# Kernel tuning notes

Measured on AMD Instinct MI355X. Metric: run time of the kernel, lower is better.

Reference implementation:

```python
import jax, jax.numpy as jnp
import numpy as np

G = 16                 # grid side -> 4096 voxels
N_GRID = G ** 3
N_NODES = 4096         # protein nodes
DEG = 256              # node neighbors per grid voxel
HID = 64               # MPNN hidden == ResNet in_channels
NUM_CLASSES = 20
BN = np.float32(1.0 / np.sqrt(1.0 + 1e-5))  # eval-mode BatchNorm3d (mean=0, var=1, gamma=1, beta=0)


def _lin(key, fi, fo):
    return jax.random.normal(key, (fi, fo), jnp.float32) * (fi ** -0.5)


def _cw(key, o, i, k):
    return jax.random.normal(key, (o, i, k, k, k), jnp.float32) * ((i * k ** 3) ** -0.5)


def setup_inputs() -> dict:
    key = jax.random.key(0)
    ks = jax.random.split(key, 32)
    n_edges = N_GRID * DEG
    # every grid voxel receives exactly DEG messages (bincount never zero)
    edge_i = jax.random.randint(ks[0], (n_edges,), 0, N_NODES, dtype=jnp.int32)
    edge_j = jnp.repeat(jnp.arange(N_GRID, dtype=jnp.int32), DEG)
    edge_index = jnp.stack([edge_i, edge_j])  # [2, E]

    node_embedding = jax.random.normal(ks[1], (N_NODES, HID), jnp.float32)
    node_pos = jax.random.uniform(ks[2], (N_NODES, 3), jnp.float32)
    gx = (jnp.arange(G, dtype=jnp.float32) + 0.5) / G
    gd, gh, gw = jnp.meshgrid(gx, gx, gx, indexing='ij')
    grid_pos = jnp.stack([gd, gh, gw], -1).reshape(N_GRID, 3)

    z = lambda n: jnp.zeros((n,), jnp.float32)
    return {
        'node_embedding': node_embedding, 'node_pos': node_pos,
        'grid_pos': grid_pos, 'edge_index': edge_index,
        # MPNN edge / message / update MLPs
        'ew1': _lin(ks[3], 6, HID), 'eb1': z(HID), 'ew2': _lin(ks[4], HID, HID), 'eb2': z(HID),
        'mw1': _lin(ks[5], 2 * HID, HID), 'mb1': z(HID), 'mw2': _lin(ks[6], HID, HID), 'mb2': z(HID),
        'uw1': _lin(ks[7], HID, HID), 'ub1': z(HID), 'uw2': _lin(ks[8], HID, HID), 'ub2': z(HID),
        # ResNet3D: 3 Blocks (conv3 a, conv3 b, conv5 shortcut) with channels 64->64, 64->128, 128->256
        'c1a': _cw(ks[9], 64, 64, 3), 'c1b': _cw(ks[10], 64, 64, 3), 'c1s': _cw(ks[11], 64, 64, 5),
        'c2a': _cw(ks[12], 128, 64, 3), 'c2b': _cw(ks[13], 128, 128, 3), 'c2s': _cw(ks[14], 128, 64, 5),
        'c3a': _cw(ks[15], 256, 128, 3), 'c3b': _cw(ks[16], 256, 256, 3), 'c3s': _cw(ks[17], 256, 128, 5),
        'fcw': _lin(ks[18], 256, NUM_CLASSES), 'fcb': z(NUM_CLASSES),
    }


def _mlp(x, w1, b1, w2, b2):
    return jax.nn.silu(x @ w1 + b1) @ w2 + b2


def _conv(x, w, p):
    return jax.lax.conv_general_dilated(
        x, w, window_strides=(1, 1, 1), padding=[(p, p)] * 3,
        dimension_numbers=('NCDHW', 'OIDHW', 'NCDHW'))


def _block(x, wa, wb, ws):
    out = jax.nn.relu(_conv(x, wa, 1) * BN)
    out = _conv(out, wb, 1) * BN
    sc = _conv(x, ws, 2) * BN
    return jax.nn.relu(out + sc)


def reference(node_embedding, node_pos, grid_pos, edge_index,
              ew1, eb1, ew2, eb2, mw1, mb1, mw2, mb2, uw1, ub1, uw2, ub2,
              c1a, c1b, c1s, c2a, c2b, c2s, c3a, c3b, c3s, fcw, fcb):
    i, j = edge_index[0], edge_index[1]
    # ---- MPNN: gather, edge MLP, message MLP, scatter-mean, update MLP ----
    edge_attr = jnp.concatenate([node_pos[i], grid_pos[j]], axis=-1)        # [E, 6]
    pos_emb = _mlp(edge_attr, ew1, eb1, ew2, eb2)                           # [E, H]
    msg = _mlp(jnp.concatenate([node_embedding[i], pos_emb], -1),
               mw1, mb1, mw2, mb2)                                          # [E, H]
    agg = jax.ops.segment_sum(msg, j, num_segments=N_GRID)                  # [N_GRID, H]
    cnt = jax.ops.segment_sum(jnp.ones((msg.shape[0],), msg.dtype), j,
                              num_segments=N_GRID)
    grid_feat = _mlp(agg / cnt[:, None], uw1, ub1, uw2, ub2)                # [N_GRID, H]
    # ---- ResNet3D over the grid volume ----
    x = grid_feat.T.reshape(1, HID, G, G, G) * BN                           # instance_norm1 (eval BN)
    x = _block(x, c1a, c1b, c1s)
    x = _block(x, c2a, c2b, c2s)
    x = _block(x, c3a, c3b, c3s)
    pooled = jnp.max(x, axis=(2, 3, 4))                                     # max_pool3d(kernel=spatial)
    return pooled @ fcw + fcb                                               # [1, NUM_CLASSES]
```

## Files before the change

kernel.cpp:

```cpp
#include <hip/hip_runtime.h>
#include <math.h>

#define BN_S 0.9999950000374997f

typedef _Float16 half8 __attribute__((ext_vector_type(8)));
typedef float f32x4 __attribute__((ext_vector_type(4)));

__device__ __forceinline__ float silu_f(float x) {
    return __fdividef(x, 1.0f + __expf(-x));
}

__device__ __forceinline__ void gld16(const void* g, void* l) {
    __builtin_amdgcn_global_load_lds(
        (const __attribute__((address_space(1))) void*)g,
        (__attribute__((address_space(3))) void*)l, 16, 0, 0);
}

__global__ __launch_bounds__(64) void prep_w_k(
    const float* __restrict__ ew2, const float* __restrict__ mw1,
    const float* __restrict__ mw2, const float* __restrict__ uw1,
    const float* __restrict__ mb2, const float* __restrict__ ub1,
    float* __restrict__ W_mu, float* __restrict__ b_mu,
    _Float16* __restrict__ wemt_h, _Float16* __restrict__ wemt_l)
{
    const int k = blockIdx.x, c = threadIdx.x;
    float s = 0.f;
    for (int m = 0; m < 64; m++) s = fmaf(ew2[k*64 + m], mw1[(64 + m)*64 + c], s);
    {
        const int q = k >> 5, kg = (k >> 3) & 3, jj = k & 7;
        const int sl = q*256 + c*4 + kg;
        const int p = sl ^ ((sl >> 3) & 7);
        const _Float16 h = (_Float16)s;
        const _Float16 l = (_Float16)(s - (float)h);
        wemt_h[p*8 + jj] = h;
        wemt_l[p*8 + jj] = l;
    }
    float s2 = 0.f;
    for (int m = 0; m < 64; m++) s2 = fmaf(mw2[k*64 + m], uw1[m*64 + c], s2);
    W_mu[k*64 + c] = s2;
    if (k == 0) {
        float s3 = ub1[c];
        for (int m = 0; m < 64; m++) s3 = fmaf(mb2[m], uw1[m*64 + c], s3);
        b_mu[c] = s3;
    }
}

__global__ __launch_bounds__(64) void prep_nodes_k(
    const float* __restrict__ node_embedding, const float* __restrict__ node_pos,
    const float* __restrict__ grid_pos, const float* __restrict__ ew1,
    const float* __restrict__ eb1, const float* __restrict__ mw1,
    const float* __restrict__ mb1, const float* __restrict__ eb2,
    float* __restrict__ a_node, float* __restrict__ g_vox, float* __restrict__ n_node)
{
    const int v = blockIdx.x, c = threadIdx.x;
    const float p0 = node_pos[v*3], p1 = node_pos[v*3 + 1], p2 = node_pos[v*3 + 2];
    a_node[v*64 + c] = fmaf(p0, ew1[c], fmaf(p1, ew1[64 + c], fmaf(p2, ew1[128 + c], eb1[c])));
    const float q0 = grid_pos[v*3], q1 = grid_pos[v*3 + 1], q2 = grid_pos[v*3 + 2];
    g_vox[v*64 + c] = fmaf(q0, ew1[192 + c], fmaf(q1, ew1[256 + c], q2 * ew1[320 + c]));
    float s = mb1[c];
    for (int k = 0; k < 64; k++) s = fmaf(node_embedding[v*64 + k], mw1[k*64 + c], s);
    for (int k = 0; k < 64; k++) s = fmaf(eb2[k], mw1[(64 + k)*64 + c], s);
    n_node[v*64 + c] = s;
}

template<int K3, int NCOG, int NCH>
__global__ __launch_bounds__(256) void wsplit_k(
    const float* __restrict__ w, _Float16* __restrict__ dh, _Float16* __restrict__ dl,
    int CI)
{
    __shared__ float s[32*K3];
    const int co = blockIdx.x, cig = blockIdx.y, t = threadIdx.x;
    const float* src = w + ((size_t)co*CI + cig*32)*K3;
    for (int m = t; m < 32*K3; m += 256) s[m] = src[m];
    __syncthreads();
    const int coG = co >> 6, col = co & 63;
    for (int m = t; m < 32*K3; m += 256) {
        const int tap = m >> 5, cil = m & 31;
        const float x = s[cil*K3 + tap];
        const _Float16 h = (_Float16)x;
        const _Float16 l = (_Float16)(x - (float)h);
        const int b = cil >> 3, jj = cil & 7;
        const int sl = col*4 + b;
        const int p = sl ^ ((sl >> 3) & 7);
        const size_t base = ((size_t)(tap*NCOG + coG)*NCH + cig) * 2048;
        dh[base + p*8 + jj] = h;
        dl[base + p*8 + jj] = l;
    }
}

__global__ __launch_bounds__(256) void edge_kernel(
    const int* __restrict__ edge_i,
    const float* __restrict__ a_node, const float* __restrict__ g_vox,
    const float* __restrict__ n_node,
    const _Float16* __restrict__ wemt_h, const _Float16* __restrict__ wemt_l,
    const float* __restrict__ W_mu, const float* __restrict__ b_mu,
    const float* __restrict__ uw2, const float* __restrict__ ub2,
    _Float16* __restrict__ x0h, _Float16* __restrict__ x0l)
{
    __shared__ __align__(16) _Float16 sAh[4096], sAl[4096];
    __shared__ __align__(16) _Float16 sBh[4096], sBl[4096];
    __shared__ float sV1[64], sV2[64];

    const int j = blockIdx.x, t = threadIdx.x;
    const int lane = t & 63, wv = t >> 6, ln15 = lane & 15, kg = lane >> 4;
    const int ebase = j << 8;

    gld16(wemt_h + t*8, &sAh[t*8]);
    gld16(wemt_h + 2048 + t*8, &sAh[2048 + t*8]);
    gld16(wemt_l + t*8, &sAl[t*8]);
    gld16(wemt_l + 2048 + t*8, &sAl[2048 + t*8]);

    const int r = t >> 2, sub = t & 3;
    float gv[16];
    #pragma unroll
    for (int m = 0; m < 16; m++) gv[m] = g_vox[j*64 + sub*16 + m];

    asm volatile("s_waitcnt vmcnt(0)" ::: "memory");
    __syncthreads();

    float psum[4] = {0.f, 0.f, 0.f, 0.f};

    for (int T = 0; T < 4; T++) {
        {
            const int i = edge_i[ebase + T*64 + r];
            float s1[16];
            #pragma unroll
            for (int m = 0; m < 16; m++)
                s1[m] = silu_f(a_node[i*64 + sub*16 + m] + gv[m]);
            half8 h0, l0, h1, l1;
            #pragma unroll
            for (int m = 0; m < 8; m++) {
                h0[m] = (_Float16)s1[m];
                l0[m] = (_Float16)(s1[m] - (float)h0[m]);
                h1[m] = (_Float16)s1[8 + m];
                l1[m] = (_Float16)(s1[8 + m] - (float)h1[m]);
            }
            const int q = sub >> 1, kg0 = (sub & 1) * 2;
            const int slot0 = (q*4 + kg0)*64 + r;
            *(half8*)&sBh[slot0*8] = h0; *(half8*)&sBl[slot0*8] = l0;
            *(half8*)&sBh[(slot0 + 64)*8] = h1; *(half8*)&sBl[(slot0 + 64)*8] = l1;
        }
        __syncthreads();
        #pragma unroll
        for (int eF = 0; eF < 4; eF++) {
            const int e = eF*16 + ln15;
            const int ie = edge_i[ebase + T*64 + e];
            f32x4 acc;
            {
                const float4 nv = *(const float4*)&n_node[(size_t)ie*64 + wv*16 + kg*4];
                acc[0] = nv.x; acc[1] = nv.y; acc[2] = nv.z; acc[3] = nv.w;
            }
            #pragma unroll
            for (int q = 0; q < 2; q++) {
                const int sa = q*256 + (wv*16 + ln15)*4 + kg;
                const int pa = sa ^ ((sa >> 3) & 7);
                const half8 Ah = *(const half8*)&sAh[pa*8];
                const half8 Al = *(const half8*)&sAl[pa*8];
                const int sb = ((q*4 + kg)*64 + e)*8;
                const half8 Bh = *(const half8*)&sBh[sb];
                const half8 Bl = *(const half8*)&sBl[sb];
                acc = __builtin_amdgcn_mfma_f32_16x16x32_f16(Ah, Bh, acc, 0, 0, 0);
                acc = __builtin_amdgcn_mfma_f32_16x16x32_f16(Ah, Bl, acc, 0, 0, 0);
                acc = __builtin_amdgcn_mfma_f32_16x16x32_f16(Al, Bh, acc, 0, 0, 0);
            }
            #pragma unroll
            for (int rg = 0; rg < 4; rg++) psum[rg] += silu_f(acc[rg]);
        }
        __syncthreads();
    }

    #pragma unroll
    for (int rg = 0; rg < 4; rg++) {
        float v = psum[rg];
        v += __shfl_xor(v, 1, 64); v += __shfl_xor(v, 2, 64);
        v += __shfl_xor(v, 4, 64); v += __shfl_xor(v, 8, 64);
        psum[rg] = v;
    }
    if (ln15 == 0) {
        #pragma unroll
        for (int rg = 0; rg < 4; rg++)
            sV1[wv*16 + kg*4 + rg] = psum[rg] * (1.0f / 256.0f);
    }
    __syncthreads();
    if (t < 64) {
        float h = b_mu[t];
        for (int k = 0; k < 64; k++) h = fmaf(sV1[k], W_mu[k*64 + t], h);
        sV2[t] = silu_f(h);
    }
    __syncthreads();
    if (t < 64) {
        float g = ub2[t];
        for (int k = 0; k < 64; k++) g = fmaf(sV2[k], uw2[k*64 + t], g);
        const float val = g * BN_S;
        const _Float16 hh = (_Float16)val;
        const _Float16 ll = (_Float16)(val - (float)hh);
        const int c = t, zz = j >> 8, v = j & 255;
        const size_t a16 = ((size_t)((c >> 5)*16 + zz)*1024 + ((c >> 3) & 3)*256 + v)*8 + (c & 7);
        x0h[a16] = hh; x0l[a16] = ll;
    }
}

template<int KK, int CI, int NCO32, int CIS>
__global__ __launch_bounds__(256) void conv_mfma_k(
    const _Float16* __restrict__ xh, const _Float16* __restrict__ xl,
    const _Float16* __restrict__ wh, const _Float16* __restrict__ wl,
    float* __restrict__ slab)
{
    constexpr int P = KK/2, K2 = KK*KK, NCH = CI/32, NCHS = NCH/CIS;
    constexpr int CO = NCO32*32, NCOG64 = NCO32/2;
    const int d0 = blockIdx.x, coG32 = blockIdx.y;
    const int co64G = coG32 >> 1, coHalf = coG32 & 1;
    const int cis = blockIdx.z / KK, kd = blockIdx.z % KK;
    const int t = threadIdx.x;
    const int lane = t & 63, wv = t >> 6;
    const int ln15 = lane & 15, kg = lane >> 4;

    float* sout = slab + ((size_t)blockIdx.z*CO + coG32*32)*4096 + d0*256;
    const int z = d0 + kd - P;
    if ((unsigned)z >= 16u) {
        for (int m = t; m < 32*256; m += 256)
            sout[(size_t)(m >> 8)*4096 + (m & 255)] = 0.f;
        return;
    }

    __shared__ __align__(16) _Float16 sXh[2][8192];
    __shared__ __align__(16) _Float16 sXl[2][8192];
    __shared__ __align__(16) _Float16 zb[8];
    if (t < 8) zb[t] = (_Float16)0.f;

    int aoff[2];
    #pragma unroll
    for (int cf = 0; cf < 2; cf++) {
        const int s = (coHalf*32 + cf*16 + ln15)*4 + kg;
        aoff[cf] = (s ^ ((s >> 3) & 7)) * 8;
    }

    auto stage_X = [&](int xb, int ch) {
        const size_t b16 = ((size_t)ch*16 + z) * 8192;
        #pragma unroll
        for (int q = 0; q < 4; q++) {
            gld16(xh + b16 + (q*256 + t)*8, &sXh[xb][(q*256 + t)*8]);
            gld16(xl + b16 + (q*256 + t)*8, &sXl[xb][(q*256 + t)*8]);
        }
    };
    auto loadA = [&](int ch, int t2, half8* Ah, half8* Al) {
        const size_t b = ((size_t)((kd*K2 + t2)*NCOG64 + co64G)*NCH + ch) * 2048;
        #pragma unroll
        for (int cf = 0; cf < 2; cf++) {
            Ah[cf] = *(const half8*)&wh[b + aoff[cf]];
            Al[cf] = *(const half8*)&wl[b + aoff[cf]];
        }
    };

    f32x4 acc[2][4];
    #pragma unroll
    for (int a = 0; a < 2; a++)
        #pragma unroll
        for (int b = 0; b < 4; b++)
            #pragma unroll
            for (int r2 = 0; r2 < 4; r2++) acc[a][b][r2] = 0.f;

    const int ch0 = cis * NCHS;
    half8 nAh[2], nAl[2];
    stage_X(0, ch0);
    loadA(ch0, 0, nAh, nAl);
    asm volatile("s_waitcnt vmcnt(0)" ::: "memory");
    __syncthreads();

    for (int cc = 0; cc < NCHS; cc++) {
        const int ch = ch0 + cc, xb = cc & 1;
        if (cc + 1 < NCHS) stage_X(xb ^ 1, ch + 1);
        for (int t2 = 0; t2 < K2; t2++) {
            half8 cAh[2], cAl[2];
            #pragma unroll
            for (int cf = 0; cf < 2; cf++) { cAh[cf] = nAh[cf]; cAl[cf] = nAl[cf]; }
            if (t2 + 1 < K2)          loadA(ch, t2 + 1, nAh, nAl);
            else if (cc + 1 < NCHS)   loadA(ch + 1, 0, nAh, nAl);

            const int kh = t2 / KK, kw = t2 % KK;
            __builtin_amdgcn_s_setprio(1);
            #pragma unroll
            for (int f = 0; f < 4; f++) {
                const int h_in = wv*4 + f + kh - P;
                if ((unsigned)h_in < 16u) {
                    const int w_in = ln15 + kw - P;
                    const bool ok = (unsigned)w_in < 16u;
                    const int slot = ok ? (kg*256 + h_in*16 + w_in) : 0;
                    const half8 Bh = ok ? *(const half8*)&sXh[xb][slot*8] : *(const half8*)zb;
                    const half8 Bl = ok ? *(const half8*)&sXl[xb][slot*8] : *(const half8*)zb;
                    #pragma unroll
                    for (int cf = 0; cf < 2; cf++) {
                        acc[cf][f] = __builtin_amdgcn_mfma_f32_16x16x32_f16(cAh[cf], Bh, acc[cf][f], 0, 0, 0);
                        acc[cf][f] = __builtin_amdgcn_mfma_f32_16x16x32_f16(cAh[cf], Bl, acc[cf][f], 0, 0, 0);
                        acc[cf][f] = __builtin_amdgcn_mfma_f32_16x16x32_f16(cAl[cf], Bh, acc[cf][f], 0, 0, 0);
                    }
                }
            }
            __builtin_amdgcn_s_setprio(0);
        }
        asm volatile("s_waitcnt vmcnt(0)" ::: "memory");
        __syncthreads();
    }

    #pragma unroll
    for (int cf = 0; cf < 2; cf++)
        #pragma unroll
        for (int f = 0; f < 4; f++)
            #pragma unroll
            for (int r2 = 0; r2 < 4; r2++)
                sout[(size_t)(cf*16 + kg*4 + r2)*4096 + wv*64 + f*16 + ln15] = acc[cf][f][r2];
}

template<int S, int RMODE, int OUT>
__global__ __launch_bounds__(256) void reduce_k(
    const float* __restrict__ pbuf, const float* __restrict__ addsrc,
    float* __restrict__ outf, _Float16* __restrict__ oh, _Float16* __restrict__ ol,
    int CO)
{
    const int z = blockIdx.x, c8 = blockIdx.y, v = threadIdx.x;
    float val[8];
    #pragma unroll
    for (int jj = 0; jj < 8; jj++) {
        const int c = c8*8 + jj;
        float a = 0.f;
        #pragma unroll
        for (int s = 0; s < S; s++)
            a += pbuf[((size_t)s*CO + c)*4096 + z*256 + v];
        a *= BN_S;
        if (RMODE == 3) a += addsrc[(size_t)c*4096 + z*256 + v];
        if (RMODE != 2) a = fmaxf(a, 0.f);
        val[jj] = a;
    }
    if (OUT == 0) {
        #pragma unroll
        for (int jj = 0; jj < 8; jj++)
            outf[(size_t)(c8*8 + jj)*4096 + z*256 + v] = val[jj];
    } else if (OUT == 1) {
        half8 hv, lv;
        #pragma unroll
        for (int jj = 0; jj < 8; jj++) {
            hv[jj] = (_Float16)val[jj];
            lv[jj] = (_Float16)(val[jj] - (float)hv[jj]);
        }
        const size_t a16 = ((size_t)((c8 >> 2)*16 + z)*1024 + (c8 & 3)*256 + v)*8;
        *(half8*)&oh[a16] = hv;
        *(half8*)&ol[a16] = lv;
    } else {
        __shared__ float sm[4][8];
        #pragma unroll
        for (int jj = 0; jj < 8; jj++) {
            float m = val[jj];
            m = fmaxf(m, __shfl_xor(m, 1, 64));  m = fmaxf(m, __shfl_xor(m, 2, 64));
            m = fmaxf(m, __shfl_xor(m, 4, 64));  m = fmaxf(m, __shfl_xor(m, 8, 64));
            m = fmaxf(m, __shfl_xor(m, 16, 64)); m = fmaxf(m, __shfl_xor(m, 32, 64));
            if ((v & 63) == 0) sm[v >> 6][jj] = m;
        }
        __syncthreads();
        if (v < 8) {
            const float m = fmaxf(fmaxf(sm[0][v], sm[1][v]), fmaxf(sm[2][v], sm[3][v]));
            outf[z*CO + c8*8 + v] = m;
        }
    }
}

__global__ __launch_bounds__(256) void fc_k(
    const float* __restrict__ pp, const float* __restrict__ fcw,
    const float* __restrict__ fcb, float* __restrict__ out)
{
    __shared__ float sp[256];
    const int t = threadIdx.x;
    float m = pp[t];
    for (int zz = 1; zz < 16; zz++) m = fmaxf(m, pp[zz*256 + t]);
    sp[t] = m;
    __syncthreads();
    if (t < 20) {
        float s = fcb[t];
        for (int c = 0; c < 256; c++) s = fmaf(sp[c], fcw[c*20 + t], s);
        out[t] = s;
    }
}

extern "C" void kernel_launch(void* const* d_in, const int* in_sizes, int n_in,
                              void* d_out, int out_size, void* d_ws, size_t ws_size,
                              hipStream_t stream)
{
    const float* node_embedding = (const float*)d_in[0];
    const float* node_pos       = (const float*)d_in[1];
    const float* grid_pos       = (const float*)d_in[2];
    const int*   edge_index     = (const int*)d_in[3];
    const float* ew1 = (const float*)d_in[4];
    const float* eb1 = (const float*)d_in[5];
    const float* ew2 = (const float*)d_in[6];
    const float* eb2 = (const float*)d_in[7];
    const float* mw1 = (const float*)d_in[8];
    const float* mb1 = (const float*)d_in[9];
    const float* mw2 = (const float*)d_in[10];
    const float* mb2 = (const float*)d_in[11];
    const float* uw1 = (const float*)d_in[12];
    const float* ub1 = (const float*)d_in[13];
    const float* uw2 = (const float*)d_in[14];
    const float* ub2 = (const float*)d_in[15];
    const float* c1a = (const float*)d_in[16];
    const float* c1b = (const float*)d_in[17];
    const float* c1s = (const float*)d_in[18];
    const float* c2a = (const float*)d_in[19];
    const float* c2b = (const float*)d_in[20];
    const float* c2s = (const float*)d_in[21];
    const float* c3a = (const float*)d_in[22];
    const float* c3b = (const float*)d_in[23];
    const float* c3s = (const float*)d_in[24];
    const float* fcw = (const float*)d_in[25];
    const float* fcb = (const float*)d_in[26];
    float* out = (float*)d_out;
    const int* edge_i = edge_index;

    float* ws = (float*)d_ws;
    float* a_node = ws;                ws += 262144;
    float* g_vox  = ws;                ws += 262144;
    float* n_node = ws;                ws += 262144;
    float* W_mu   = ws;                ws += 4096;
    float* b_mu   = ws;                ws += 64;
    _Float16* wemt_h = (_Float16*)ws;  ws += 2048;
    _Float16* wemt_l = (_Float16*)ws;  ws += 2048;
    _Float16* x0h = (_Float16*)ws;     ws += 131072;
    _Float16* x0l = (_Float16*)ws;     ws += 131072;
    _Float16* t2h = (_Float16*)ws;     ws += 262144;
    _Float16* t2l = (_Float16*)ws;     ws += 262144;
    _Float16* x2h = (_Float16*)ws;     ws += 262144;
    _Float16* x2l = (_Float16*)ws;     ws += 262144;
    _Float16* t3h = (_Float16*)ws;     ws += 524288;
    _Float16* t3l = (_Float16*)ws;     ws += 524288;
    float* u2 = ws;                    ws += 524288;
    float* u3 = ws;                    ws += 1048576;
    float* slab = ws;                  ws += 5242880;
    float* poolPart = ws;              ws += 4096;
    _Float16* wh = (_Float16*)ws;      ws += 4585472;
    _Float16* wl = (_Float16*)ws;      ws += 4585472;
    _Float16* t1h = (_Float16*)a_node;
    _Float16* t1l = (_Float16*)(a_node + 131072);
    float* u1 = g_vox;
    _Float16* x1h = (_Float16*)n_node;
    _Float16* x1l = (_Float16*)(n_node + 131072);

    _Float16* w1a_h = wh + 0;       _Float16* w1a_l = wl + 0;
    _Float16* w1b_h = wh + 110592;  _Float16* w1b_l = wl + 110592;
    _Float16* w1s_h = wh + 221184;  _Float16* w1s_l = wl + 221184;
    _Float16* w2a_h = wh + 733184;  _Float16* w2a_l = wl + 733184;
    _Float16* w2b_h = wh + 954368;  _Float16* w2b_l = wl + 954368;
    _Float16* w2s_h = wh + 1396736; _Float16* w2s_l = wl + 1396736;
    _Float16* w3a_h = wh + 2420736; _Float16* w3a_l = wl + 2420736;
    _Float16* w3b_h = wh + 3305472; _Float16* w3b_l = wl + 3305472;
    _Float16* w3s_h = wh + 5074944; _Float16* w3s_l = wl + 5074944;

    hipLaunchKernelGGL((wsplit_k<27,1,2>),  dim3(64,2),  dim3(256), 0, stream, c1a, w1a_h, w1a_l, 64);
    hipLaunchKernelGGL((wsplit_k<27,1,2>),  dim3(64,2),  dim3(256), 0, stream, c1b, w1b_h, w1b_l, 64);
    hipLaunchKernelGGL((wsplit_k<125,1,2>), dim3(64,2),  dim3(256), 0, stream, c1s, w1s_h, w1s_l, 64);
    hipLaunchKernelGGL((wsplit_k<27,2,2>),  dim3(128,2), dim3(256), 0, stream, c2a, w2a_h, w2a_l, 64);
    hipLaunchKernelGGL((wsplit_k<27,2,4>),  dim3(128,4), dim3(256), 0, stream, c2b, w2b_h, w2b_l, 128);
    hipLaunchKernelGGL((wsplit_k<125,2,2>), dim3(128,2), dim3(256), 0, stream, c2s, w2s_h, w2s_l, 64);
    hipLaunchKernelGGL((wsplit_k<27,4,4>),  dim3(256,4), dim3(256), 0, stream, c3a, w3a_h, w3a_l, 128);
    hipLaunchKernelGGL((wsplit_k<27,4,8>),  dim3(256,8), dim3(256), 0, stream, c3b, w3b_h, w3b_l, 256);
    hipLaunchKernelGGL((wsplit_k<125,4,4>), dim3(256,4), dim3(256), 0, stream, c3s, w3s_h, w3s_l, 128);

    hipLaunchKernelGGL(prep_w_k, dim3(64), dim3(64), 0, stream,
                       ew2, mw1, mw2, uw1, mb2, ub1, W_mu, b_mu, wemt_h, wemt_l);
    hipLaunchKernelGGL(prep_nodes_k, dim3(4096), dim3(64), 0, stream,
                       node_embedding, node_pos, grid_pos, ew1, eb1, mw1, mb1, eb2,
                       a_node, g_vox, n_node);
    hipLaunchKernelGGL(edge_kernel, dim3(4096), dim3(256), 0, stream,
                       edge_i, a_node, g_vox, n_node, wemt_h, wemt_l,
                       W_mu, b_mu, uw2, ub2, x0h, x0l);

    hipLaunchKernelGGL((conv_mfma_k<3,64,2,2>), dim3(16,2,6), dim3(256), 0, stream, x0h, x0l, w1a_h, w1a_l, slab);
    hipLaunchKernelGGL((reduce_k<6,1,1>), dim3(16,8), dim3(256), 0, stream, slab, (const float*)nullptr, (float*)nullptr, t1h, t1l, 64);
    hipLaunchKernelGGL((conv_mfma_k<3,64,2,2>), dim3(16,2,6), dim3(256), 0, stream, t1h, t1l, w1b_h, w1b_l, slab);
    hipLaunchKernelGGL((reduce_k<6,2,0>), dim3(16,8), dim3(256), 0, stream, slab, (const float*)nullptr, u1, (_Float16*)nullptr, (_Float16*)nullptr, 64);
    hipLaunchKernelGGL((conv_mfma_k<5,64,2,2>), dim3(16,2,10), dim3(256), 0, stream, x0h, x0l, w1s_h, w1s_l, slab);
    hipLaunchKernelGGL((reduce_k<10,3,1>), dim3(16,8), dim3(256), 0, stream, slab, u1, (float*)nullptr, x1h, x1l, 64);
    hipLaunchKernelGGL((conv_mfma_k<3,64,4,2>), dim3(16,4,6), dim3(256), 0, stream, x1h, x1l, w2a_h, w2a_l, slab);
    hipLaunchKernelGGL((reduce_k<6,1,1>), dim3(16,16), dim3(256), 0, stream, slab, (const float*)nullptr, (float*)nullptr, t2h, t2l, 128);
    hipLaunchKernelGGL((conv_mfma_k<3,128,4,2>), dim3(16,4,6), dim3(256), 0, stream, t2h, t2l, w2b_h, w2b_l, slab);
    hipLaunchKernelGGL((reduce_k<6,2,0>), dim3(16,16), dim3(256), 0, stream, slab, (const float*)nullptr, u2, (_Float16*)nullptr, (_Float16*)nullptr, 128);
    hipLaunchKernelGGL((conv_mfma_k<5,64,4,2>), dim3(16,4,10), dim3(256), 0, stream, x1h, x1l, w2s_h, w2s_l, slab);
    hipLaunchKernelGGL((reduce_k<10,3,1>), dim3(16,16), dim3(256), 0, stream, slab, u2, (float*)nullptr, x2h, x2l, 128);
    hipLaunchKernelGGL((conv_mfma_k<3,128,8,1>), dim3(16,8,3), dim3(256), 0, stream, x2h, x2l, w3a_h, w3a_l, slab);
    hipLaunchKernelGGL((reduce_k<3,1,1>), dim3(16,32), dim3(256), 0, stream, slab, (const float*)nullptr, (float*)nullptr, t3h, t3l, 256);
    hipLaunchKernelGGL((conv_mfma_k<3,256,8,1>), dim3(16,8,3), dim3(256), 0, stream, t3h, t3l, w3b_h, w3b_l, slab);
    hipLaunchKernelGGL((reduce_k<3,2,0>), dim3(16,32), dim3(256), 0, stream, slab, (const float*)nullptr, u3, (_Float16*)nullptr, (_Float16*)nullptr, 256);
    hipLaunchKernelGGL((conv_mfma_k<5,128,8,1>), dim3(16,8,5), dim3(256), 0, stream, x2h, x2l, w3s_h, w3s_l, slab);
    hipLaunchKernelGGL((reduce_k<5,3,2>), dim3(16,32), dim3(256), 0, stream, slab, u3, poolPart, (_Float16*)nullptr, (_Float16*)nullptr, 256);

    hipLaunchKernelGGL(fc_k, dim3(1), dim3(256), 0, stream, poolPart, fcw, fcb, out);

    (void)in_sizes; (void)n_in; (void)out_size; (void)ws_size;
}
```

Before: 521.0 us.

## Single-buffer conv input tile, XOR-swizzle activation layout, raise occupancy hint

The conv kernel's input staging goes from double-buffered to single-buffered LDS, which halves shared memory per block. It also adds a launch_bounds occupancy hint of 4 blocks per CU so more blocks can be resident. Producers of the fp16 hi/lo activations now write with an XOR swizzle of the voxel index keyed by channel octet, and the B-fragment reads undo it, to cut LDS bank conflicts. The cost is that loading the next channel chunk no longer overlaps compute and needs an extra barrier, relying on higher occupancy to hide that latency.

```diff
diff --git a/kernel.cpp b/kernel.cpp
--- a/kernel.cpp
+++ b/kernel.cpp
@@ -195,13 +195,15 @@
         const _Float16 hh = (_Float16)val;
         const _Float16 ll = (_Float16)(val - (float)hh);
         const int c = t, zz = j >> 8, v = j & 255;
-        const size_t a16 = ((size_t)((c >> 5)*16 + zz)*1024 + ((c >> 3) & 3)*256 + v)*8 + (c & 7);
+        const int oct = (c >> 3) & 3;
+        const int vsw = v ^ (oct << 1);
+        const size_t a16 = ((size_t)((c >> 5)*16 + zz)*1024 + oct*256 + vsw)*8 + (c & 7);
         x0h[a16] = hh; x0l[a16] = ll;
     }
 }
 
 template<int KK, int CI, int NCO32, int CIS>
-__global__ __launch_bounds__(256) void conv_mfma_k(
+__global__ __launch_bounds__(256, 4) void conv_mfma_k(
     const _Float16* __restrict__ xh, const _Float16* __restrict__ xl,
     const _Float16* __restrict__ wh, const _Float16* __restrict__ wl,
     float* __restrict__ slab)
@@ -223,8 +225,8 @@
         return;
     }
 
-    __shared__ __align__(16) _Float16 sXh[2][8192];
-    __shared__ __align__(16) _Float16 sXl[2][8192];
+    __shared__ __align__(16) _Float16 sXh[8192];
+    __shared__ __align__(16) _Float16 sXl[8192];
     __shared__ __align__(16) _Float16 zb[8];
     if (t < 8) zb[t] = (_Float16)0.f;
 
@@ -235,12 +237,12 @@
         aoff[cf] = (s ^ ((s >> 3) & 7)) * 8;
     }
 
-    auto stage_X = [&](int xb, int ch) {
+    auto stage_X = [&](int ch) {
         const size_t b16 = ((size_t)ch*16 + z) * 8192;
         #pragma unroll
         for (int q = 0; q < 4; q++) {
-            gld16(xh + b16 + (q*256 + t)*8, &sXh[xb][(q*256 + t)*8]);
-            gld16(xl + b16 + (q*256 + t)*8, &sXl[xb][(q*256 + t)*8]);
+            gld16(xh + b16 + (q*256 + t)*8, &sXh[(q*256 + t)*8]);
+            gld16(xl + b16 + (q*256 + t)*8, &sXl[(q*256 + t)*8]);
         }
     };
     auto loadA = [&](int ch, int t2, half8* Ah, half8* Al) {
@@ -262,14 +264,13 @@
 
     const int ch0 = cis * NCHS;
     half8 nAh[2], nAl[2];
-    stage_X(0, ch0);
+    stage_X(ch0);
     loadA(ch0, 0, nAh, nAl);
     asm volatile("s_waitcnt vmcnt(0)" ::: "memory");
     __syncthreads();
 
     for (int cc = 0; cc < NCHS; cc++) {
-        const int ch = ch0 + cc, xb = cc & 1;
-        if (cc + 1 < NCHS) stage_X(xb ^ 1, ch + 1);
+        const int ch = ch0 + cc;
         for (int t2 = 0; t2 < K2; t2++) {
             half8 cAh[2], cAl[2];
             #pragma unroll
@@ -285,9 +286,9 @@
                 if ((unsigned)h_in < 16u) {
                     const int w_in = ln15 + kw - P;
                     const bool ok = (unsigned)w_in < 16u;
-                    const int slot = ok ? (kg*256 + h_in*16 + w_in) : 0;
-                    const half8 Bh = ok ? *(const half8*)&sXh[xb][slot*8] : *(const half8*)zb;
-                    const half8 Bl = ok ? *(const half8*)&sXl[xb][slot*8] : *(const half8*)zb;
+                    const int slot = ok ? (kg*256 + h_in*16 + (w_in ^ (kg << 1))) : 0;
+                    const half8 Bh = ok ? *(const half8*)&sXh[slot*8] : *(const half8*)zb;
+                    const half8 Bl = ok ? *(const half8*)&sXl[slot*8] : *(const half8*)zb;
                     #pragma unroll
                     for (int cf = 0; cf < 2; cf++) {
                         acc[cf][f] = __builtin_amdgcn_mfma_f32_16x16x32_f16(cAh[cf], Bh, acc[cf][f], 0, 0, 0);
@@ -298,8 +299,12 @@
             }
             __builtin_amdgcn_s_setprio(0);
         }
-        asm volatile("s_waitcnt vmcnt(0)" ::: "memory");
-        __syncthreads();
+        if (cc + 1 < NCHS) {
+            __syncthreads();
+            stage_X(ch + 1);
+            asm volatile("s_waitcnt vmcnt(0)" ::: "memory");
+            __syncthreads();
+        }
     }
 
     #pragma unroll
@@ -342,7 +347,9 @@
             hv[jj] = (_Float16)val[jj];
             lv[jj] = (_Float16)(val[jj] - (float)hv[jj]);
         }
-        const size_t a16 = ((size_t)((c8 >> 2)*16 + z)*1024 + (c8 & 3)*256 + v)*8;
+        const int oct = c8 & 3;
+        const int vsw = v ^ (oct << 1);
+        const size_t a16 = ((size_t)((c8 >> 2)*16 + z)*1024 + oct*256 + vsw)*8;
         *(half8*)&oh[a16] = hv;
         *(half8*)&ol[a16] = lv;
     } else {
```

Measured after the change: 538.4 us. 3.3% more time.
